# Kernel optimization log

Measured on AMD Instinct MI355X. Metric: run time of the kernel, lower is better.

The kernel has to match this reference:

```python
import jax, jax.numpy as jnp
import numpy as np

B, L, D, H, K, F, M = 4, 384, 512, 8, 64, 2048, 512
NL, NCT, ND = 2, 6, 15
BINS = jnp.arange(10, 150, 10, dtype=jnp.float32)  # 14 boundaries -> 15 buckets
EPS = 1e-5


def _ln(x, g, b):
    mu = x.mean(-1, keepdims=True)
    v = ((x - mu) ** 2).mean(-1, keepdims=True)
    return (x - mu) / jnp.sqrt(v + EPS) * g + b


def _attn(x, didx, dr, mask, de, Wq, bq, Wk, bk, Wv, bv, Wo, bo):
    # x: [B,L,D]; didx: [B,L,L] distance bucket ids; dr: [B,L] dist-to-responder ids
    Q = (x @ Wq + bq).reshape(B, L, H, K)
    Kh = (x @ Wk + bk).reshape(B, L, H, K)
    V = (x @ Wv + bv).reshape(B, L, H, K)
    # NOTE: original module computes sqrt_K but never divides by it (faithful).
    E = jnp.einsum('blhk,bxhk->bhlx', Q, Kh)
    E = E + jnp.einsum('blhk,blxk->bhlx', Q, de[0][didx])          # Kqk term
    E = E + jnp.einsum('blhk,blk->bhl', Q, de[1][dr])[..., None]    # Kqr term (const over keys)
    E = E + jnp.einsum('blhk,bxk->bhlx', Q, de[2][dr])              # Kkr term
    # faithful replication of torch's mask.repeat(1,H,1,L).reshape(B,H,L,L)
    mask4 = jnp.tile(mask[None, None, :, :], (1, H, 1, L)).reshape(B, H, L, L)
    E = jnp.where(mask4 == 0, -jnp.inf, E)
    A = jax.nn.softmax(E, axis=-1)                                  # [B,H,L,L]
    Z = jnp.einsum('bhlx,bxhk->blhk', A, V)
    Z = Z + jnp.einsum('bhlx,blxk->blhk', A, de[3][didx])           # Vqk term
    Z = Z + de[4][dr][:, :, None, :]                                 # Vqr term (broadcast over heads)
    Z = Z + jnp.einsum('bhlx,bxk->blhk', A, de[5][dr])              # Vkr term
    return Z.reshape(B, L, D) @ Wo + bo


def _forward(cell_types_BL, distances_BLL, padding_mask_BL, cell_emb, dist_emb,
             Wq, bq, Wk, bk, Wv, bv, Wo, bo, W1, b1, W2, b2,
             g1, be1, g2, be2, Wm1, bm1, Wm2, bm2):
    h = cell_emb[cell_types_BL]                                      # [B,L,D]
    # torch.bucketize(right=False) == searchsorted side='left'
    didx = jnp.searchsorted(BINS, distances_BLL, side='left')        # [B,L,L]
    dr = didx[:, 0]                                                  # RESPONDER_CELL_IDX = 0
    for l in range(NL):
        a = _attn(h, didx, dr, padding_mask_BL, dist_emb,
                  Wq[l], bq[l], Wk[l], bk[l], Wv[l], bv[l], Wo[l], bo[l])
        h = _ln(h + a, g1[l], be1[l])                                # post-norm
        ff = jax.nn.gelu(h @ W1[l] + b1[l], approximate=False) @ W2[l] + b2[l]
        h = _ln(h + ff, g2[l], be2[l])
    pooled = jnp.einsum('bld,bl->bd', h, padding_mask_BL)            # mask-weighted sum pool
    return jax.nn.relu(pooled @ Wm1 + bm1) @ Wm2 + bm2               # [B,1]


def setup_inputs() -> dict:
    key = jax.random.key(0)
    ks = list(jax.random.split(key, 32))
    it = iter(ks)

    def nrm(shape, scale=0.02):
        return jax.random.normal(next(it), shape, dtype=jnp.float32) * scale

    return {
        'cell_types_BL': jax.random.randint(next(it), (B, L), 0, NCT),
        'distances_BLL': jax.random.uniform(next(it), (B, L, L), dtype=jnp.float32) * 160.0,
        'padding_mask_BL': jnp.ones((B, L), dtype=jnp.float32),
        'cell_emb': nrm((NCT, D), 1.0),
        'dist_emb': nrm((6, ND, K), 1.0),  # order: Kqk,Kqr,Kkr,Vqk,Vqr,Vkr
        'Wq': nrm((NL, D, D)), 'bq': jnp.zeros((NL, D)),
        'Wk': nrm((NL, D, D)), 'bk': jnp.zeros((NL, D)),
        'Wv': nrm((NL, D, D)), 'bv': jnp.zeros((NL, D)),
        'Wo': nrm((NL, D, D)), 'bo': jnp.zeros((NL, D)),
        'W1': nrm((NL, D, F)), 'b1': jnp.zeros((NL, F)),
        'W2': nrm((NL, F, D)), 'b2': jnp.zeros((NL, D)),
        'g1': jnp.ones((NL, D)), 'be1': jnp.zeros((NL, D)),
        'g2': jnp.ones((NL, D)), 'be2': jnp.zeros((NL, D)),
        'Wm1': nrm((D, M)), 'bm1': jnp.zeros((M,)),
        'Wm2': nrm((M, 1)), 'bm2': jnp.zeros((1,)),
    }


def reference(cell_types_BL, distances_BLL, padding_mask_BL, cell_emb, dist_emb,
              Wq, bq, Wk, bk, Wv, bv, Wo, bo, W1, b1, W2, b2,
              g1, be1, g2, be2, Wm1, bm1, Wm2, bm2):
    return _forward(cell_types_BL, distances_BLL, padding_mask_BL, cell_emb, dist_emb,
                    Wq, bq, Wk, bk, Wv, bv, Wo, bo, W1, b1, W2, b2,
                    g1, be1, g2, be2, Wm1, bm1, Wm2, bm2)
```

## Files before the change

kernel.cpp:

```cpp
#include <hip/hip_runtime.h>
#include <math.h>

#define Bb 4
#define Lq 384
#define Dm 512
#define Hh 8
#define Kk 64
#define Ff 2048
#define Mm 512
#define NLAY 2
#define NDb 15
#define BL (Bb*Lq)
#define QKVLD 1536
#define KeROWS 448
#define EP 460
#define PPs 920
#define LWP 17
#define QR 16

typedef __attribute__((ext_vector_type(8))) short bfrag;
typedef __attribute__((ext_vector_type(4))) float f32x4;
typedef __attribute__((ext_vector_type(4))) short short4v;
typedef __attribute__((ext_vector_type(2))) unsigned int uint2v;
typedef unsigned int uint;
typedef unsigned char uchar;

__device__ __forceinline__ short f2b(float f) {
    unsigned u = __builtin_bit_cast(unsigned, f);
    unsigned r = (u + 0x7fffu + ((u >> 16) & 1u)) >> 16;
    return (short)r;
}
__device__ __forceinline__ float b2f(short s) {
    unsigned u = ((unsigned)(unsigned short)s) << 16;
    return __builtin_bit_cast(float, u);
}

__device__ __forceinline__ void tile_tr(const float* __restrict__ src, short* __restrict__ dst,
                                        int Kd, int N, int t, int tx, int ty) {
    __shared__ float ts[32][33];
    int nt = t % (N / 32), kt = t / (N / 32);
    int n0 = nt * 32, k0 = kt * 32;
    for (int i = ty; i < 32; i += 8) ts[i][tx] = src[(size_t)(k0 + i) * N + n0 + tx];
    __syncthreads();
    for (int i = ty; i < 32; i += 8) dst[(size_t)(n0 + i) * Kd + k0 + tx] = f2b(ts[tx][i]);
}

__global__ __launch_bounds__(256) void prologue_all(
        const int* __restrict__ ct, const float* __restrict__ cell_emb,
        const float* __restrict__ dist, const float* __restrict__ de,
        const float* __restrict__ bq, const float* __restrict__ bk, const float* __restrict__ bv,
        const float* __restrict__ Wq, const float* __restrict__ Wk,
        const float* __restrict__ Wv, const float* __restrict__ Wo,
        const float* __restrict__ W1, const float* __restrict__ W2,
        const float* __restrict__ Wm1,
        float* __restrict__ h, short* __restrict__ hb,
        uchar* __restrict__ didx8, int* __restrict__ dr, float* __restrict__ qkvb,
        short* __restrict__ Ke, short* __restrict__ Wt_all, short* __restrict__ Wm1T) {
    const size_t WLAY = 4ull * Dm * Dm + (size_t)Dm * Ff + (size_t)Ff * Dm;
    int blk = blockIdx.x, tid = threadIdx.x;
    if (blk < 576) {
        int i = blk * 256 + tid;
        f32x4 d = *(const f32x4*)(dist + (size_t)i * 4);
        uint r = 0;
#pragma unroll
        for (int c = 0; c < 4; ++c) {
            int cnt = 0;
#pragma unroll
            for (int q = 1; q <= 14; ++q) cnt += (float)(10 * q) < d[c] ? 1 : 0;
            r |= (uint)cnt << (8 * c);
        }
        ((uint*)didx8)[i] = r;
    } else if (blk < 582) {
        int i = (blk - 576) * 256 + tid;
        if (i < BL) {
            int b = i / Lq, x = i % Lq;
            float d = dist[(size_t)b * Lq * Lq + x];
            int c = 0;
#pragma unroll
            for (int q = 1; q <= 14; ++q) c += (float)(10 * q) < d ? 1 : 0;
            dr[i] = c;
        }
    } else if (blk < 3654) {
        int i = (blk - 582) * 256 + tid;
        int row = i / Dm, d = i % Dm;
        float v = cell_emb[ct[row] * Dm + d];
        h[i] = v;
        hb[i] = f2b(v);
    } else if (blk < 3666) {
        int i = (blk - 3654) * 256 + tid;
        int l = i / QKVLD, c = i % QKVLD;
        float v = (c < Dm) ? bq[l * Dm + c] : (c < 2 * Dm) ? bk[l * Dm + c - Dm] : bv[l * Dm + c - 2 * Dm];
        qkvb[i] = v;
    } else if (blk < 4178) {
        int i = (blk - 3666) * 256 + tid;
        int k = i & 63, rr = (i >> 6) & 63, z = i >> 12;
        short v = (rr < NDb) ? f2b(de[rr * Kk + k]) : (short)0;
        Ke[((size_t)z * KeROWS + Lq + rr) * Kk + k] = v;
    } else {
        int idx = blk - 4178;
        int tx = tid & 31, ty = tid >> 5;
        if (idx < 2048) {
            int m4 = idx >> 9, rem = idx & 511, l = rem >> 8, t = rem & 255;
            const float* src = (m4 == 0 ? Wq : m4 == 1 ? Wk : m4 == 2 ? Wv : Wo) + (size_t)l * Dm * Dm;
            tile_tr(src, Wt_all + l * WLAY + (size_t)m4 * Dm * Dm, Dm, Dm, t, tx, ty);
        } else if (idx < 4096) {
            int rem = idx - 2048, l = rem >> 10, t = rem & 1023;
            tile_tr(W1 + (size_t)l * Dm * Ff, Wt_all + l * WLAY + 4ull * Dm * Dm, Dm, Ff, t, tx, ty);
        } else if (idx < 6144) {
            int rem = idx - 4096, l = rem >> 10, t = rem & 1023;
            tile_tr(W2 + (size_t)l * Ff * Dm, Wt_all + l * WLAY + 4ull * Dm * Dm + (size_t)Dm * Ff, Ff, Dm, t, tx, ty);
        } else {
            tile_tr(Wm1, Wm1T, Dm, Mm, idx - 6144, tx, ty);
        }
    }
}

__global__ __launch_bounds__(128) void qkv_gemm(const short* __restrict__ A,
                                                const short* __restrict__ Bt,
                                                const float* __restrict__ bias,
                                                const int* __restrict__ dr,
                                                const float* __restrict__ de,
                                                short* __restrict__ Qb,
                                                short* __restrict__ Ke,
                                                short* __restrict__ Vet) {
    const int tid = threadIdx.x;
    const int wave = tid >> 6, lane = tid & 63;
    const int row0 = blockIdx.y * 32, col0 = blockIdx.x * 64;
    const int r = lane & 15, g = lane >> 4;
    const int kbase = wave * (Dm / 2);
    __shared__ float red[64][33];
    f32x4 acc[2][4] = {};
#pragma unroll 4
    for (int k0 = 0; k0 < Dm / 2; k0 += 32) {
        bfrag a[2], b[4];
#pragma unroll
        for (int i = 0; i < 2; ++i)
            a[i] = *(const bfrag*)(A + (size_t)(row0 + i * 16 + r) * Dm + kbase + k0 + g * 8);
#pragma unroll
        for (int j = 0; j < 4; ++j)
            b[j] = *(const bfrag*)(Bt + (size_t)(col0 + j * 16 + r) * Dm + kbase + k0 + g * 8);
#pragma unroll
        for (int i = 0; i < 2; ++i)
#pragma unroll
            for (int j = 0; j < 4; ++j)
                acc[i][j] = __builtin_amdgcn_mfma_f32_16x16x32_bf16(a[i], b[j], acc[i][j], 0, 0, 0);
    }
    if (wave == 1) {
#pragma unroll
        for (int i = 0; i < 2; ++i)
#pragma unroll
            for (int j = 0; j < 4; ++j)
#pragma unroll
                for (int v = 0; v < 4; ++v)
                    red[lane][(i * 4 + j) * 4 + v] = acc[i][j][v];
    }
    __syncthreads();
    if (wave != 0) return;
#pragma unroll
    for (int i = 0; i < 2; ++i)
#pragma unroll
        for (int j = 0; j < 4; ++j)
#pragma unroll
            for (int v = 0; v < 4; ++v)
                acc[i][j][v] += red[lane][(i * 4 + j) * 4 + v];
    const float* de2 = de + 2 * NDb * Kk;
    const float* de5 = de + 5 * NDb * Kk;
#pragma unroll
    for (int i = 0; i < 2; ++i)
#pragma unroll
        for (int v = 0; v < 4; ++v) {
            int row = row0 + i * 16 + g * 4 + v;
            int b = row / Lq, x = row - b * Lq;
            int dd = dr[row];
#pragma unroll
            for (int j = 0; j < 4; ++j) {
                int col = col0 + j * 16 + r;
                float val = acc[i][j][v] + bias[col];
                if (col < Dm) {
                    Qb[(size_t)row * Dm + col] = f2b(val);
                } else {
                    int k = col & 63, h2 = (col >> 6) & 7, z = b * Hh + h2;
                    if (col < 2 * Dm)
                        Ke[((size_t)z * KeROWS + x) * Kk + k] = f2b(val + de2[dd * Kk + k]);
                    else
                        Vet[((size_t)z * Kk + k) * Lq + x] = f2b(val + de5[dd * Kk + k]);
                }
            }
        }
}

__global__ __launch_bounds__(256) void attn_fused(const short* __restrict__ Qb,
                                                  const short* __restrict__ Ke,
                                                  const short* __restrict__ Vet,
                                                  const uchar* __restrict__ didx8,
                                                  const int* __restrict__ dr,
                                                  const float* __restrict__ de,
                                                  short* __restrict__ Zb) {
    const int n = blockIdx.x;
    const int xcd = n & 7, kblk = n >> 3;
    const int z = xcd * 4 + (kblk & 3);
    const int qt = kblk >> 2;
    const int b = z >> 3, hh = z & 7;
    const int tid = threadIdx.x;
    const int wave = tid >> 6, lane = tid & 63;
    const int r = lane & 15, g = lane >> 4;
    __shared__ float Ef[QR * EP];
    __shared__ float lw[QR * LWP];
    __shared__ float invrow[QR];

    const int row = tid >> 4, s16 = tid & 15;
    const int grow = qt * QR + row;
    const uchar* dxp = didx8 + ((size_t)(b * Lq + grow)) * Lq + s16 * 24;
    uint2v w0 = *(const uint2v*)(dxp);
    uint2v w1 = *(const uint2v*)(dxp + 8);
    uint2v w2 = *(const uint2v*)(dxp + 16);

    const short* Qbase = Qb + ((size_t)(b * Lq + qt * QR)) * Dm + hh * Kk;
    const short* Kbase = Ke + (size_t)z * KeROWS * Kk;
    f32x4 eacc[4][2] = {};
#pragma unroll
    for (int k0 = 0; k0 < Kk; k0 += 32) {
        bfrag a = *(const bfrag*)(Qbase + (size_t)r * Dm + k0 + g * 8);
#pragma unroll
        for (int t = 0; t < 4; ++t) {
            int ctile = wave + t * 4;
            if (ctile < 14) {
                bfrag bb[2];
#pragma unroll
                for (int i = 0; i < 2; ++i)
                    bb[i] = *(const bfrag*)(Kbase + (size_t)(ctile * 32 + i * 16 + r) * Kk + k0 + g * 8);
#pragma unroll
                for (int j = 0; j < 2; ++j)
                    eacc[t][j] = __builtin_amdgcn_mfma_f32_16x16x32_bf16(a, bb[j], eacc[t][j], 0, 0, 0);
            }
        }
    }
#pragma unroll
    for (int t = 0; t < 4; ++t) {
        int ctile = wave + t * 4;
        if (ctile < 14) {
#pragma unroll
            for (int j = 0; j < 2; ++j)
#pragma unroll
                for (int v = 0; v < 4; ++v)
                    Ef[(g * 4 + v) * EP + ctile * 32 + j * 16 + r] = eacc[t][j][v];
        }
    }
    __syncthreads();

    float* Er = Ef + row * EP;
    uint dxw[6] = {w0[0], w0[1], w1[0], w1[1], w2[0], w2[1]};
    float sv[24];
    float mx = -1e30f;
#pragma unroll
    for (int u = 0; u < 6; ++u) {
        f32x4 ev = *(const f32x4*)(Er + s16 * 24 + u * 4);
        uint w = dxw[u];
#pragma unroll
        for (int c = 0; c < 4; ++c) {
            int dxv = (w >> (8 * c)) & 255;
            float s = ev[c] + Er[Lq + dxv];
            sv[u * 4 + c] = s;
            mx = fmaxf(mx, s);
        }
    }
    mx = fmaxf(mx, __shfl_xor(mx, 1));
    mx = fmaxf(mx, __shfl_xor(mx, 2));
    mx = fmaxf(mx, __shfl_xor(mx, 4));
    mx = fmaxf(mx, __shfl_xor(mx, 8));
    float sum = 0.f;
    float bins[NDb];
#pragma unroll
    for (int q = 0; q < NDb; ++q) bins[q] = 0.f;
#pragma unroll
    for (int u = 0; u < 6; ++u) {
        uint w = dxw[u];
#pragma unroll
        for (int c = 0; c < 4; ++c) {
            int dxv = (w >> (8 * c)) & 255;
            float e = __expf(sv[u * 4 + c] - mx);
            sv[u * 4 + c] = e;
            sum += e;
#pragma unroll
            for (int q = 0; q < NDb; ++q) bins[q] += (dxv == q) ? e : 0.f;
        }
    }
    sum += __shfl_xor(sum, 1);
    sum += __shfl_xor(sum, 2);
    sum += __shfl_xor(sum, 4);
    sum += __shfl_xor(sum, 8);
#pragma unroll
    for (int q = 0; q < NDb; ++q) {
        bins[q] += __shfl_xor(bins[q], 1);
        bins[q] += __shfl_xor(bins[q], 2);
        bins[q] += __shfl_xor(bins[q], 4);
        bins[q] += __shfl_xor(bins[q], 8);
    }
    float inv = 1.0f / sum;
    if (s16 == 0) {
        invrow[row] = inv;
#pragma unroll
        for (int q = 0; q < NDb; ++q) lw[row * LWP + q] = bins[q];
    }
    uint pk[12];
#pragma unroll
    for (int i = 0; i < 12; ++i) {
        uint lo = (unsigned short)f2b(sv[2 * i] * inv);
        uint hi = (unsigned short)f2b(sv[2 * i + 1] * inv);
        pk[i] = lo | (hi << 16);
    }
    __syncthreads();
    uint* prow = (uint*)((short*)Ef + row * PPs + s16 * 24);
#pragma unroll
    for (int i = 0; i < 12; ++i) prow[i] = pk[i];
    __syncthreads();

    const short* Ps = (const short*)Ef;
    const short* brow = Vet + (size_t)z * Kk * Lq + (size_t)(wave * 16 + r) * Lq;
    f32x4 pacc = {};
#pragma unroll
    for (int k0 = 0; k0 < Lq; k0 += 32) {
        bfrag bb = *(const bfrag*)(brow + k0 + g * 8);
        bfrag a = *(const bfrag*)(Ps + (size_t)r * PPs + k0 + g * 8);
        pacc = __builtin_amdgcn_mfma_f32_16x16x32_bf16(a, bb, pacc, 0, 0, 0);
    }
    const float* de3 = de + 3 * NDb * Kk;
    const float* de4 = de + 4 * NDb * Kk;
    const int k = wave * 16 + r;
    float d3[NDb];
#pragma unroll
    for (int q = 0; q < NDb; ++q) d3[q] = de3[q * Kk + k];
#pragma unroll
    for (int v = 0; v < 4; ++v) {
        int lrow = g * 4 + v;
        int gr = qt * QR + lrow;
        float wsv = 0.f;
#pragma unroll
        for (int q = 0; q < NDb; ++q) wsv += lw[lrow * LWP + q] * d3[q];
        int dd = dr[b * Lq + gr];
        float val = pacc[v] + wsv * invrow[lrow] + de4[dd * Kk + k];
        Zb[((size_t)(b * Lq + gr)) * Dm + hh * Kk + k] = f2b(val);
    }
}

template <int ACT, int OUTBF, int KD, int CT, int KW>
__global__ __launch_bounds__(64 * KW) void mfma_gemm(const short* __restrict__ A,
                                                     const short* __restrict__ Bt,
                                                     const float* __restrict__ bias,
                                                     void* __restrict__ Cv,
                                                     int lda, int ldb, int ldc) {
    const int tid = threadIdx.x;
    const int wave = tid >> 6, lane = tid & 63;
    const int row0 = blockIdx.y * 32, col0 = blockIdx.x * (16 * CT);
    const int r = lane & 15, g = lane >> 4;
    const int KC = KD / KW;
    const int kbase = wave * KC;
    __shared__ float red[KW > 1 ? KW - 1 : 1][64][2 * CT * 4 + 1];
    f32x4 acc[2][CT] = {};
#pragma unroll 4
    for (int k0 = 0; k0 < KC; k0 += 32) {
        bfrag a[2], b[CT];
#pragma unroll
        for (int i = 0; i < 2; ++i)
            a[i] = *(const bfrag*)(A + (size_t)(row0 + i * 16 + r) * lda + kbase + k0 + g * 8);
#pragma unroll
        for (int j = 0; j < CT; ++j)
            b[j] = *(const bfrag*)(Bt + (size_t)(col0 + j * 16 + r) * ldb + kbase + k0 + g * 8);
#pragma unroll
        for (int i = 0; i < 2; ++i)
#pragma unroll
            for (int j = 0; j < CT; ++j)
                acc[i][j] = __builtin_amdgcn_mfma_f32_16x16x32_bf16(a[i], b[j], acc[i][j], 0, 0, 0);
    }
    if (KW > 1) {
        if (wave > 0) {
#pragma unroll
            for (int i = 0; i < 2; ++i)
#pragma unroll
                for (int j = 0; j < CT; ++j)
#pragma unroll
                    for (int v = 0; v < 4; ++v)
                        red[wave - 1][lane][(i * CT + j) * 4 + v] = acc[i][j][v];
        }
        __syncthreads();
        if (wave != 0) return;
#pragma unroll
        for (int w = 0; w < KW - 1; ++w)
#pragma unroll
            for (int i = 0; i < 2; ++i)
#pragma unroll
                for (int j = 0; j < CT; ++j)
#pragma unroll
                    for (int v = 0; v < 4; ++v)
                        acc[i][j][v] += red[w][lane][(i * CT + j) * 4 + v];
    }
#pragma unroll
    for (int i = 0; i < 2; ++i)
#pragma unroll
        for (int j = 0; j < CT; ++j)
#pragma unroll
            for (int v = 0; v < 4; ++v) {
                int row = row0 + i * 16 + g * 4 + v;
                int col = col0 + j * 16 + r;
                float val = acc[i][j][v] + bias[col];
                if (ACT == 1) val = 0.5f * val * (1.0f + erff(val * 0.7071067811865475f));
                if (OUTBF) ((short*)Cv)[(size_t)row * ldc + col] = f2b(val);
                else       ((float*)Cv)[(size_t)row * ldc + col] = val;
            }
}

__global__ __launch_bounds__(128) void add_ln_kernel(float* __restrict__ h,
                                                     short* __restrict__ hb,
                                                     const float* __restrict__ delta,
                                                     const float* __restrict__ g,
                                                     const float* __restrict__ be) {
    const int row = blockIdx.x, t = threadIdx.x;
    const int lane = t & 63, wid = t >> 6;
    __shared__ float red[4];
    f32x4 x = *(const f32x4*)(h + (size_t)row * Dm + t * 4);
    f32x4 d = *(const f32x4*)(delta + (size_t)row * Dm + t * 4);
    x = x + d;
    float s = x[0] + x[1] + x[2] + x[3];
#pragma unroll
    for (int o = 32; o >= 1; o >>= 1) s += __shfl_xor(s, o);
    if (lane == 0) red[wid] = s;
    __syncthreads();
    float mu = (red[0] + red[1]) * (1.0f / 512.0f);
    f32x4 dif;
    float vs = 0.f;
#pragma unroll
    for (int c = 0; c < 4; ++c) { dif[c] = x[c] - mu; vs += dif[c] * dif[c]; }
#pragma unroll
    for (int o = 32; o >= 1; o >>= 1) vs += __shfl_xor(vs, o);
    if (lane == 0) red[wid + 2] = vs;
    __syncthreads();
    float rstd = rsqrtf((red[2] + red[3]) * (1.0f / 512.0f) + 1e-5f);
    f32x4 gg = *(const f32x4*)(g + t * 4);
    f32x4 bb = *(const f32x4*)(be + t * 4);
    f32x4 y;
    short4v yb;
#pragma unroll
    for (int c = 0; c < 4; ++c) { y[c] = dif[c] * rstd * gg[c] + bb[c]; yb[c] = f2b(y[c]); }
    *(f32x4*)(h + (size_t)row * Dm + t * 4) = y;
    *(short4v*)(hb + (size_t)row * Dm + t * 4) = yb;
}

__global__ __launch_bounds__(512) void pool_partial(const float* __restrict__ h,
                                                    const float* __restrict__ mask,
                                                    float* __restrict__ partial) {
    int c = blockIdx.x, b = blockIdx.y, d = threadIdx.x;
    float acc = 0.f;
#pragma unroll 8
    for (int i = 0; i < 64; ++i) {
        int l = c * 64 + i;
        acc += h[((size_t)(b * Lq + l)) * Dm + d] * mask[b * Lq + l];
    }
    partial[((size_t)(b * 6 + c)) * Dm + d] = acc;
}

__global__ __launch_bounds__(256) void head_mlp(const float* __restrict__ partial,
                                                const short* __restrict__ Wm1T,
                                                const float* __restrict__ bm1,
                                                const float* __restrict__ Wm2,
                                                float* __restrict__ mlp_t) {
    int w = blockIdx.x * 4 + (threadIdx.x >> 6);
    int lane = threadIdx.x & 63;
    int m = w >> 2, b = w & 3;
    const short* wr = Wm1T + (size_t)m * Dm;
    float acc = 0.f;
#pragma unroll
    for (int i = 0; i < 8; ++i) {
        int k = lane * 8 + i;
        float pool = 0.f;
#pragma unroll
        for (int c = 0; c < 6; ++c) pool += partial[((size_t)(b * 6 + c)) * Dm + k];
        acc += pool * b2f(wr[k]);
    }
#pragma unroll
    for (int off = 32; off >= 1; off >>= 1) acc += __shfl_xor(acc, off);
    if (lane == 0) mlp_t[b * Mm + m] = fmaxf(acc + bm1[m], 0.f) * Wm2[m];
}

__global__ __launch_bounds__(256) void final_kernel(const float* __restrict__ mlp_t,
                                                    const float* __restrict__ bm2,
                                                    float* __restrict__ out) {
    int b = blockIdx.x, t = threadIdx.x;
    int lane = t & 63, wid = t >> 6;
    __shared__ float red[4];
    float v = mlp_t[b * Mm + t] + mlp_t[b * Mm + 256 + t];
#pragma unroll
    for (int off = 32; off >= 1; off >>= 1) v += __shfl_xor(v, off);
    if (lane == 0) red[wid] = v;
    __syncthreads();
    if (t == 0) out[b] = red[0] + red[1] + red[2] + red[3] + bm2[0];
}

extern "C" void kernel_launch(void* const* d_in, const int* in_sizes, int n_in,
                              void* d_out, int out_size, void* d_ws, size_t ws_size,
                              hipStream_t stream) {
    const int* ct        = (const int*)d_in[0];
    const float* dist    = (const float*)d_in[1];
    const float* mask    = (const float*)d_in[2];
    const float* cellemb = (const float*)d_in[3];
    const float* de      = (const float*)d_in[4];
    const float* Wq = (const float*)d_in[5];
    const float* bq = (const float*)d_in[6];
    const float* Wk = (const float*)d_in[7];
    const float* bk = (const float*)d_in[8];
    const float* Wv = (const float*)d_in[9];
    const float* bv = (const float*)d_in[10];
    const float* Wo = (const float*)d_in[11];
    const float* bo = (const float*)d_in[12];
    const float* W1 = (const float*)d_in[13];
    const float* b1 = (const float*)d_in[14];
    const float* W2 = (const float*)d_in[15];
    const float* b2 = (const float*)d_in[16];
    const float* g1 = (const float*)d_in[17];
    const float* be1 = (const float*)d_in[18];
    const float* g2 = (const float*)d_in[19];
    const float* be2 = (const float*)d_in[20];
    const float* Wm1 = (const float*)d_in[21];
    const float* bm1 = (const float*)d_in[22];
    const float* Wm2 = (const float*)d_in[23];
    const float* bm2 = (const float*)d_in[24];
    float* out = (float*)d_out;

    float* ws = (float*)d_ws;
    float* h       = ws;
    float* tmp     = h + (size_t)BL * Dm;
    float* qkvb    = tmp + (size_t)BL * Dm;
    float* partial = qkvb + NLAY * QKVLD;
    float* mlp_t   = partial + (size_t)Bb * 6 * Dm;
    int* dr        = (int*)(mlp_t + Bb * Mm);
    uchar* didx8   = (uchar*)(dr + Bb * Lq);
    short* hb      = (short*)(didx8 + (size_t)Bb * Lq * Lq);
    short* Qb      = hb + (size_t)BL * Dm;
    short* Zb      = Qb + (size_t)BL * Dm;
    short* ffb     = Zb + (size_t)BL * Dm;
    short* Wt_all  = ffb + (size_t)BL * Ff;
    const size_t WLAY = 4ull * Dm * Dm + (size_t)Dm * Ff + (size_t)Ff * Dm;
    short* Wm1T    = Wt_all + NLAY * WLAY;
    short* Ke      = Wm1T + (size_t)Mm * Dm;
    short* Vet     = Ke + (size_t)Bb * Hh * KeROWS * Kk;

    prologue_all<<<10578, 256, 0, stream>>>(ct, cellemb, dist, de, bq, bk, bv,
                                            Wq, Wk, Wv, Wo, W1, W2, Wm1,
                                            h, hb, didx8, dr, qkvb, Ke, Wt_all, Wm1T);

    dim3 gQKV(QKVLD / 64, BL / 32);
    dim3 gD(Dm / 32, BL / 32);
    dim3 gF(Ff / 64, BL / 32);

    for (int l = 0; l < NLAY; ++l) {
        short* base = Wt_all + l * WLAY;
        short* WoT = base + 3 * Dm * Dm;
        short* W1T = base + 4 * Dm * Dm;
        short* W2T = base + 4 * Dm * Dm + Dm * Ff;

        qkv_gemm<<<gQKV, 128, 0, stream>>>(hb, base, qkvb + l * QKVLD, dr, de, Qb, Ke, Vet);
        attn_fused<<<768, 256, 0, stream>>>(Qb, Ke, Vet, didx8, dr, de, Zb);

        mfma_gemm<0, 0, Dm, 2, 2><<<gD, 128, 0, stream>>>(Zb, WoT, bo + l * Dm, tmp, Dm, Dm, Dm);
        add_ln_kernel<<<BL, 128, 0, stream>>>(h, hb, tmp, g1 + l * Dm, be1 + l * Dm);

        mfma_gemm<1, 1, Dm, 4, 2><<<gF, 128, 0, stream>>>(hb, W1T, b1 + l * Ff, ffb, Dm, Dm, Ff);
        mfma_gemm<0, 0, Ff, 2, 4><<<gD, 256, 0, stream>>>(ffb, W2T, b2 + l * Dm, tmp, Ff, Ff, Dm);
        add_ln_kernel<<<BL, 128, 0, stream>>>(h, hb, tmp, g2 + l * Dm, be2 + l * Dm);
    }

    pool_partial<<<dim3(6, Bb), 512, 0, stream>>>(h, mask, partial);
    head_mlp<<<512, 256, 0, stream>>>(partial, Wm1T, bm1, Wm2, mlp_t);
    final_kernel<<<Bb, 256, 0, stream>>>(mlp_t, bm2, out);
}
```

Before: 239.5 us.

## Fuse residual add and LayerNorm into the following GEMM prologues

Removes three of the four standalone add+LayerNorm kernels. Each consuming GEMM (FFN1 and the layer-2 QKV projection) now computes per-row mean and rstd from the residual plus delta, then builds normalized bf16 A-fragments on the fly, and its column-0 blocks write the fp32 hidden state. Ping-pong hidden buffers avoid read/write races, and the layer loop is unrolled. In exchange, every column block recomputes the row statistics and re-reads two fp32 tensors instead of one bf16 tensor. The variance now uses E[x^2]-mu^2, which is slightly less numerically robust.

```diff
diff --git a/kernel.cpp b/kernel.cpp
--- a/kernel.cpp
+++ b/kernel.cpp
@@ -115,6 +115,72 @@
     }
 }
 
+__device__ __forceinline__ void ln_stats(const float* __restrict__ tmpA,
+                                         const float* __restrict__ hIn,
+                                         int row0, int tid,
+                                         float* __restrict__ smu, float* __restrict__ srs) {
+    int sr = tid >> 2, sc = tid & 3;
+    const float* tr = tmpA + (size_t)(row0 + sr) * Dm;
+    const float* hr = hIn + (size_t)(row0 + sr) * Dm;
+    float s = 0.f, ss = 0.f;
+    for (int c = sc * 128; c < sc * 128 + 128; c += 4) {
+        f32x4 a = *(const f32x4*)(tr + c);
+        f32x4 b = *(const f32x4*)(hr + c);
+#pragma unroll
+        for (int j = 0; j < 4; ++j) { float x = a[j] + b[j]; s += x; ss += x * x; }
+    }
+    s += __shfl_xor(s, 1); s += __shfl_xor(s, 2);
+    ss += __shfl_xor(ss, 1); ss += __shfl_xor(ss, 2);
+    if (sc == 0) {
+        float mu = s * (1.0f / 512.0f);
+        smu[sr] = mu;
+        srs[sr] = rsqrtf(ss * (1.0f / 512.0f) - mu * mu + 1e-5f);
+    }
+}
+
+__device__ __forceinline__ void ln_write(const float* __restrict__ tmpA,
+                                         const float* __restrict__ hIn,
+                                         const float* __restrict__ gw,
+                                         const float* __restrict__ be,
+                                         int row0, int tid,
+                                         const float* __restrict__ smu,
+                                         const float* __restrict__ srs,
+                                         float* __restrict__ hOut) {
+    int sr = tid >> 2, sc = tid & 3;
+    float mu = smu[sr], rs = srs[sr];
+    const float* tr = tmpA + (size_t)(row0 + sr) * Dm;
+    const float* hr = hIn + (size_t)(row0 + sr) * Dm;
+    float* orow = hOut + (size_t)(row0 + sr) * Dm;
+    for (int c = sc * 128; c < sc * 128 + 128; c += 4) {
+        f32x4 a = *(const f32x4*)(tr + c);
+        f32x4 b = *(const f32x4*)(hr + c);
+        f32x4 gg = *(const f32x4*)(gw + c);
+        f32x4 bb = *(const f32x4*)(be + c);
+        f32x4 y;
+#pragma unroll
+        for (int j = 0; j < 4; ++j) y[j] = (a[j] + b[j] - mu) * rs * gg[j] + bb[j];
+        *(f32x4*)(orow + c) = y;
+    }
+}
+
+__device__ __forceinline__ bfrag ln_frag(const float* __restrict__ tmpA,
+                                         const float* __restrict__ hIn,
+                                         int row, int kk,
+                                         float mu, float rs,
+                                         f32x4 gg0, f32x4 gg1, f32x4 bb0, f32x4 bb1) {
+    const float* tr = tmpA + (size_t)row * Dm + kk;
+    const float* hr = hIn + (size_t)row * Dm + kk;
+    f32x4 x0 = *(const f32x4*)tr + *(const f32x4*)hr;
+    f32x4 x1 = *(const f32x4*)(tr + 4) + *(const f32x4*)(hr + 4);
+    bfrag a;
+#pragma unroll
+    for (int j = 0; j < 4; ++j) {
+        a[j]     = f2b((x0[j] - mu) * rs * gg0[j] + bb0[j]);
+        a[j + 4] = f2b((x1[j] - mu) * rs * gg1[j] + bb1[j]);
+    }
+    return a;
+}
+
 __global__ __launch_bounds__(128) void qkv_gemm(const short* __restrict__ A,
                                                 const short* __restrict__ Bt,
                                                 const float* __restrict__ bias,
@@ -189,6 +255,164 @@
         }
 }
 
+__global__ __launch_bounds__(128) void qkv_gemm_ln(const float* __restrict__ tmpA,
+                                                   const float* __restrict__ hIn,
+                                                   const float* __restrict__ gw,
+                                                   const float* __restrict__ be,
+                                                   float* __restrict__ hOut,
+                                                   const short* __restrict__ Bt,
+                                                   const float* __restrict__ bias,
+                                                   const int* __restrict__ dr,
+                                                   const float* __restrict__ de,
+                                                   short* __restrict__ Qb,
+                                                   short* __restrict__ Ke,
+                                                   short* __restrict__ Vet) {
+    const int tid = threadIdx.x;
+    const int wave = tid >> 6, lane = tid & 63;
+    const int row0 = blockIdx.y * 32, col0 = blockIdx.x * 64;
+    const int r = lane & 15, g = lane >> 4;
+    const int kbase = wave * (Dm / 2);
+    __shared__ float red[64][33];
+    __shared__ float smu[32], srs[32];
+    ln_stats(tmpA, hIn, row0, tid, smu, srs);
+    __syncthreads();
+    if (blockIdx.x == 0) ln_write(tmpA, hIn, gw, be, row0, tid, smu, srs, hOut);
+    f32x4 acc[2][4] = {};
+#pragma unroll 4
+    for (int k0 = 0; k0 < Dm / 2; k0 += 32) {
+        int kk = kbase + k0 + g * 8;
+        f32x4 gg0 = *(const f32x4*)(gw + kk), gg1 = *(const f32x4*)(gw + kk + 4);
+        f32x4 bb0 = *(const f32x4*)(be + kk), bb1 = *(const f32x4*)(be + kk + 4);
+        bfrag a[2], b[4];
+#pragma unroll
+        for (int i = 0; i < 2; ++i) {
+            int row = row0 + i * 16 + r;
+            a[i] = ln_frag(tmpA, hIn, row, kk, smu[i * 16 + r], srs[i * 16 + r], gg0, gg1, bb0, bb1);
+        }
+#pragma unroll
+        for (int j = 0; j < 4; ++j)
+            b[j] = *(const bfrag*)(Bt + (size_t)(col0 + j * 16 + r) * Dm + kk);
+#pragma unroll
+        for (int i = 0; i < 2; ++i)
+#pragma unroll
+            for (int j = 0; j < 4; ++j)
+                acc[i][j] = __builtin_amdgcn_mfma_f32_16x16x32_bf16(a[i], b[j], acc[i][j], 0, 0, 0);
+    }
+    if (wave == 1) {
+#pragma unroll
+        for (int i = 0; i < 2; ++i)
+#pragma unroll
+            for (int j = 0; j < 4; ++j)
+#pragma unroll
+                for (int v = 0; v < 4; ++v)
+                    red[lane][(i * 4 + j) * 4 + v] = acc[i][j][v];
+    }
+    __syncthreads();
+    if (wave != 0) return;
+#pragma unroll
+    for (int i = 0; i < 2; ++i)
+#pragma unroll
+        for (int j = 0; j < 4; ++j)
+#pragma unroll
+            for (int v = 0; v < 4; ++v)
+                acc[i][j][v] += red[lane][(i * 4 + j) * 4 + v];
+    const float* de2 = de + 2 * NDb * Kk;
+    const float* de5 = de + 5 * NDb * Kk;
+#pragma unroll
+    for (int i = 0; i < 2; ++i)
+#pragma unroll
+        for (int v = 0; v < 4; ++v) {
+            int row = row0 + i * 16 + g * 4 + v;
+            int b = row / Lq, x = row - b * Lq;
+            int dd = dr[row];
+#pragma unroll
+            for (int j = 0; j < 4; ++j) {
+                int col = col0 + j * 16 + r;
+                float val = acc[i][j][v] + bias[col];
+                if (col < Dm) {
+                    Qb[(size_t)row * Dm + col] = f2b(val);
+                } else {
+                    int k = col & 63, h2 = (col >> 6) & 7, z = b * Hh + h2;
+                    if (col < 2 * Dm)
+                        Ke[((size_t)z * KeROWS + x) * Kk + k] = f2b(val + de2[dd * Kk + k]);
+                    else
+                        Vet[((size_t)z * Kk + k) * Lq + x] = f2b(val + de5[dd * Kk + k]);
+                }
+            }
+        }
+}
+
+__global__ __launch_bounds__(128) void ffn1_ln(const float* __restrict__ tmpA,
+                                               const float* __restrict__ hIn,
+                                               const float* __restrict__ gw,
+                                               const float* __restrict__ be,
+                                               float* __restrict__ hOut,
+                                               const short* __restrict__ Bt,
+                                               const float* __restrict__ bias,
+                                               short* __restrict__ ffb) {
+    const int tid = threadIdx.x;
+    const int wave = tid >> 6, lane = tid & 63;
+    const int row0 = blockIdx.y * 32, col0 = blockIdx.x * 64;
+    const int r = lane & 15, g = lane >> 4;
+    const int kbase = wave * (Dm / 2);
+    __shared__ float red[64][33];
+    __shared__ float smu[32], srs[32];
+    ln_stats(tmpA, hIn, row0, tid, smu, srs);
+    __syncthreads();
+    if (blockIdx.x == 0) ln_write(tmpA, hIn, gw, be, row0, tid, smu, srs, hOut);
+    f32x4 acc[2][4] = {};
+#pragma unroll 4
+    for (int k0 = 0; k0 < Dm / 2; k0 += 32) {
+        int kk = kbase + k0 + g * 8;
+        f32x4 gg0 = *(const f32x4*)(gw + kk), gg1 = *(const f32x4*)(gw + kk + 4);
+        f32x4 bb0 = *(const f32x4*)(be + kk), bb1 = *(const f32x4*)(be + kk + 4);
+        bfrag a[2], b[4];
+#pragma unroll
+        for (int i = 0; i < 2; ++i) {
+            int row = row0 + i * 16 + r;
+            a[i] = ln_frag(tmpA, hIn, row, kk, smu[i * 16 + r], srs[i * 16 + r], gg0, gg1, bb0, bb1);
+        }
+#pragma unroll
+        for (int j = 0; j < 4; ++j)
+            b[j] = *(const bfrag*)(Bt + (size_t)(col0 + j * 16 + r) * Dm + kk);
+#pragma unroll
+        for (int i = 0; i < 2; ++i)
+#pragma unroll
+            for (int j = 0; j < 4; ++j)
+                acc[i][j] = __builtin_amdgcn_mfma_f32_16x16x32_bf16(a[i], b[j], acc[i][j], 0, 0, 0);
+    }
+    if (wave == 1) {
+#pragma unroll
+        for (int i = 0; i < 2; ++i)
+#pragma unroll
+            for (int j = 0; j < 4; ++j)
+#pragma unroll
+                for (int v = 0; v < 4; ++v)
+                    red[lane][(i * 4 + j) * 4 + v] = acc[i][j][v];
+    }
+    __syncthreads();
+    if (wave != 0) return;
+#pragma unroll
+    for (int i = 0; i < 2; ++i)
+#pragma unroll
+        for (int j = 0; j < 4; ++j)
+#pragma unroll
+            for (int v = 0; v < 4; ++v)
+                acc[i][j][v] += red[lane][(i * 4 + j) * 4 + v];
+#pragma unroll
+    for (int i = 0; i < 2; ++i)
+#pragma unroll
+        for (int j = 0; j < 4; ++j)
+#pragma unroll
+            for (int v = 0; v < 4; ++v) {
+                int row = row0 + i * 16 + g * 4 + v;
+                int col = col0 + j * 16 + r;
+                float val = acc[i][j][v] + bias[col];
+                val = 0.5f * val * (1.0f + erff(val * 0.7071067811865475f));
+                ffb[(size_t)row * Ff + col] = f2b(val);
+            }
+}
+
 __global__ __launch_bounds__(256) void attn_fused(const short* __restrict__ Qb,
                                                   const short* __restrict__ Ke,
                                                   const short* __restrict__ Vet,
@@ -409,15 +633,15 @@
             }
 }
 
-__global__ __launch_bounds__(128) void add_ln_kernel(float* __restrict__ h,
-                                                     short* __restrict__ hb,
-                                                     const float* __restrict__ delta,
-                                                     const float* __restrict__ g,
-                                                     const float* __restrict__ be) {
+__global__ __launch_bounds__(128) void add_ln_final(const float* __restrict__ hIn,
+                                                    const float* __restrict__ delta,
+                                                    const float* __restrict__ g,
+                                                    const float* __restrict__ be,
+                                                    float* __restrict__ hOut) {
     const int row = blockIdx.x, t = threadIdx.x;
     const int lane = t & 63, wid = t >> 6;
     __shared__ float red[4];
-    f32x4 x = *(const f32x4*)(h + (size_t)row * Dm + t * 4);
+    f32x4 x = *(const f32x4*)(hIn + (size_t)row * Dm + t * 4);
     f32x4 d = *(const f32x4*)(delta + (size_t)row * Dm + t * 4);
     x = x + d;
     float s = x[0] + x[1] + x[2] + x[3];
@@ -438,11 +662,9 @@
     f32x4 gg = *(const f32x4*)(g + t * 4);
     f32x4 bb = *(const f32x4*)(be + t * 4);
     f32x4 y;
-    short4v yb;
-#pragma unroll
-    for (int c = 0; c < 4; ++c) { y[c] = dif[c] * rstd * gg[c] + bb[c]; yb[c] = f2b(y[c]); }
-    *(f32x4*)(h + (size_t)row * Dm + t * 4) = y;
-    *(short4v*)(hb + (size_t)row * Dm + t * 4) = yb;
+#pragma unroll
+    for (int c = 0; c < 4; ++c) y[c] = dif[c] * rstd * gg[c] + bb[c];
+    *(f32x4*)(hOut + (size_t)row * Dm + t * 4) = y;
 }
 
 __global__ __launch_bounds__(512) void pool_partial(const float* __restrict__ h,
@@ -526,9 +748,11 @@
     float* out = (float*)d_out;
 
     float* ws = (float*)d_ws;
-    float* h       = ws;
-    float* tmp     = h + (size_t)BL * Dm;
-    float* qkvb    = tmp + (size_t)BL * Dm;
+    float* hA      = ws;
+    float* hB      = hA + (size_t)BL * Dm;
+    float* tmp     = hB + (size_t)BL * Dm;
+    float* tmp2    = tmp + (size_t)BL * Dm;
+    float* qkvb    = tmp2 + (size_t)BL * Dm;
     float* partial = qkvb + NLAY * QKVLD;
     float* mlp_t   = partial + (size_t)Bb * 6 * Dm;
     int* dr        = (int*)(mlp_t + Bb * Mm);
@@ -545,30 +769,40 @@
 
     prologue_all<<<10578, 256, 0, stream>>>(ct, cellemb, dist, de, bq, bk, bv,
                                             Wq, Wk, Wv, Wo, W1, W2, Wm1,
-                                            h, hb, didx8, dr, qkvb, Ke, Wt_all, Wm1T);
+                                            hA, hb, didx8, dr, qkvb, Ke, Wt_all, Wm1T);
 
     dim3 gQKV(QKVLD / 64, BL / 32);
     dim3 gD(Dm / 32, BL / 32);
     dim3 gF(Ff / 64, BL / 32);
 
-    for (int l = 0; l < NLAY; ++l) {
-        short* base = Wt_all + l * WLAY;
+    {
+        short* base = Wt_all;
         short* WoT = base + 3 * Dm * Dm;
         short* W1T = base + 4 * Dm * Dm;
         short* W2T = base + 4 * Dm * Dm + Dm * Ff;
 
-        qkv_gemm<<<gQKV, 128, 0, stream>>>(hb, base, qkvb + l * QKVLD, dr, de, Qb, Ke, Vet);
+        qkv_gemm<<<gQKV, 128, 0, stream>>>(hb, base, qkvb, dr, de, Qb, Ke, Vet);
         attn_fused<<<768, 256, 0, stream>>>(Qb, Ke, Vet, didx8, dr, de, Zb);
-
-        mfma_gemm<0, 0, Dm, 2, 2><<<gD, 128, 0, stream>>>(Zb, WoT, bo + l * Dm, tmp, Dm, Dm, Dm);
-        add_ln_kernel<<<BL, 128, 0, stream>>>(h, hb, tmp, g1 + l * Dm, be1 + l * Dm);
-
-        mfma_gemm<1, 1, Dm, 4, 2><<<gF, 128, 0, stream>>>(hb, W1T, b1 + l * Ff, ffb, Dm, Dm, Ff);
-        mfma_gemm<0, 0, Ff, 2, 4><<<gD, 256, 0, stream>>>(ffb, W2T, b2 + l * Dm, tmp, Ff, Ff, Dm);
-        add_ln_kernel<<<BL, 128, 0, stream>>>(h, hb, tmp, g2 + l * Dm, be2 + l * Dm);
-    }
-
-    pool_partial<<<dim3(6, Bb), 512, 0, stream>>>(h, mask, partial);
+        mfma_gemm<0, 0, Dm, 2, 2><<<gD, 128, 0, stream>>>(Zb, WoT, bo, tmp, Dm, Dm, Dm);
+        ffn1_ln<<<gF, 128, 0, stream>>>(tmp, hA, g1, be1, hB, W1T, b1, ffb);
+        mfma_gemm<0, 0, Ff, 2, 4><<<gD, 256, 0, stream>>>(ffb, W2T, b2, tmp2, Ff, Ff, Dm);
+    }
+    {
+        short* base = Wt_all + WLAY;
+        short* WoT = base + 3 * Dm * Dm;
+        short* W1T = base + 4 * Dm * Dm;
+        short* W2T = base + 4 * Dm * Dm + Dm * Ff;
+
+        qkv_gemm_ln<<<gQKV, 128, 0, stream>>>(tmp2, hB, g2, be2, hA,
+                                              base, qkvb + QKVLD, dr, de, Qb, Ke, Vet);
+        attn_fused<<<768, 256, 0, stream>>>(Qb, Ke, Vet, didx8, dr, de, Zb);
+        mfma_gemm<0, 0, Dm, 2, 2><<<gD, 128, 0, stream>>>(Zb, WoT, bo + Dm, tmp, Dm, Dm, Dm);
+        ffn1_ln<<<gF, 128, 0, stream>>>(tmp, hA, g1 + Dm, be1 + Dm, hB, W1T, b1 + Ff, ffb);
+        mfma_gemm<0, 0, Ff, 2, 4><<<gD, 256, 0, stream>>>(ffb, W2T, b2 + Dm, tmp2, Ff, Ff, Dm);
+    }
+    add_ln_final<<<BL, 128, 0, stream>>>(hB, tmp2, g2 + Dm, be2 + Dm, hA);
+
+    pool_partial<<<dim3(6, Bb), 512, 0, stream>>>(hA, mask, partial);
     head_mlp<<<512, 256, 0, stream>>>(partial, Wm1T, bm1, Wm2, mlp_t);
     final_kernel<<<Bb, 256, 0, stream>>>(mlp_t, bm2, out);
 }
```

New measurement: 495.9 us. +107.1%, slower.
